# Kernel tuning notes

Measured on AMD Instinct MI355X. Metric: run time of the kernel, lower is better.

## Reference

```python
import jax, jax.numpy as jnp
import numpy as np

N_NODES = 100000
N_EDGES = 1600000
N_GRAPHS = 5000
NODE_DIM = 16
EDGE_DIM = 16
HID = 20


def setup_inputs() -> dict:
    key = jax.random.key(0)
    ks = jax.random.split(key, 12)
    edge_index = jax.random.randint(ks[0], (2, N_EDGES), 0, N_NODES)
    node_attr = jax.random.normal(ks[1], (N_NODES, NODE_DIM), dtype=jnp.float32)
    edge_attr = jax.random.normal(ks[2], (N_EDGES, EDGE_DIM), dtype=jnp.float32)
    batch = jnp.sort(jax.random.randint(ks[3], (N_NODES,), 0, N_GRAPHS))
    s = 0.1
    W_msg = jax.random.normal(ks[4], (2 * NODE_DIM + EDGE_DIM, HID), dtype=jnp.float32) * s
    b_msg = jnp.zeros((HID,), dtype=jnp.float32)
    W1 = jax.random.normal(ks[5], (HID, 10), dtype=jnp.float32) * s
    b1 = jnp.zeros((10,), dtype=jnp.float32)
    W2 = jax.random.normal(ks[6], (10, 10), dtype=jnp.float32) * s
    b2 = jnp.zeros((10,), dtype=jnp.float32)
    W3 = jax.random.normal(ks[7], (10, 1), dtype=jnp.float32) * s
    b3 = jnp.zeros((1,), dtype=jnp.float32)
    return {"edge_index": edge_index, "node_attr": node_attr, "edge_attr": edge_attr,
            "batch": batch, "W_msg": W_msg, "b_msg": b_msg, "W1": W1, "b1": b1,
            "W2": W2, "b2": b2, "W3": W3, "b3": b3}


def reference(edge_index, node_attr, edge_attr, batch,
              W_msg, b_msg, W1, b1, W2, b2, W3, b3):
    src, dst = edge_index[0], edge_index[1]
    # MPL_1: gather -> linear -> relu -> scatter-sum to destination nodes
    feats = jnp.concatenate([node_attr[src], node_attr[dst], edge_attr], axis=-1)  # [E, 48]
    msg = jax.nn.relu(feats @ W_msg + b_msg)  # [E, 20]
    x = jax.ops.segment_sum(msg, dst, num_segments=N_NODES)  # [N, 20]
    # node MLP + graph pooling (segment_coo sum over batch) + graph MLP
    x = jax.nn.relu(x @ W1 + b1)  # [N, 10]
    g = jax.ops.segment_sum(x, batch, num_segments=N_GRAPHS)  # [G, 10]
    g = jax.nn.relu(g @ W2 + b2)
    return g @ W3 + b3  # [G, 1]
```

## Files before the change

### kernel.cpp

```cpp
#include <hip/hip_runtime.h>

constexpr int NN = 100000;
constexpr int NE = 1600000;
constexpr int NG = 5000;
constexpr int BKT = 64;
constexpr int NBKT = (NN + BKT - 1) / BKT;
constexpr int NB = 128;
constexpr int CHUNK = NE / NB;

typedef float v2f __attribute__((ext_vector_type(2)));

constexpr size_t OFF_G  = 0;
constexpr size_t OFF_BH = 50048;
constexpr size_t OFF_ST = OFF_BH + (size_t)NB * NBKT;
constexpr size_t OFF_PM = OFF_ST + NBKT + 1;

__global__ __launch_bounds__(256) void k_hist(const int* __restrict__ ei,
                                              int* __restrict__ bh,
                                              float* __restrict__ g) {
  __shared__ int lh[NBKT];
  for (int i = threadIdx.x; i < NBKT; i += 256) lh[i] = 0;
  __syncthreads();
  const int* dstp = ei + NE;
  int s = blockIdx.x * CHUNK;
  for (int i = s + threadIdx.x; i < s + CHUNK; i += 256)
    atomicAdd(&lh[dstp[i] >> 6], 1);
  int gid = blockIdx.x * 256 + threadIdx.x;
  if (gid < 12500) ((float4*)g)[gid] = make_float4(0.f, 0.f, 0.f, 0.f);
  __syncthreads();
  int* out = bh + (size_t)blockIdx.x * NBKT;
  for (int k = threadIdx.x; k < NBKT; k += 256) out[k] = lh[k];
}

__global__ __launch_bounds__(256) void k_btot(const int* __restrict__ bh,
                                              int* __restrict__ starts) {
  int k = blockIdx.x * 256 + threadIdx.x;
  if (k >= NBKT) return;
  int tot = 0;
  for (int b = 0; b < NB; b += 4) {
    int a0 = bh[(size_t)(b    ) * NBKT + k];
    int a1 = bh[(size_t)(b + 1) * NBKT + k];
    int a2 = bh[(size_t)(b + 2) * NBKT + k];
    int a3 = bh[(size_t)(b + 3) * NBKT + k];
    tot += a0 + a1 + a2 + a3;
  }
  starts[k] = tot;
}

__global__ __launch_bounds__(1024) void k_sscan(int* __restrict__ starts) {
  __shared__ int s0[1024], s1[1024];
  int t = threadIdx.x;
  int k0 = 2 * t, k1 = 2 * t + 1;
  int tot0 = (k0 < NBKT) ? starts[k0] : 0;
  int tot1 = (k1 < NBKT) ? starts[k1] : 0;
  int ssum = tot0 + tot1;
  int* cur = s0; int* nxt = s1;
  cur[t] = ssum;
  __syncthreads();
  for (int off = 1; off < 1024; off <<= 1) {
    int v = cur[t];
    if (t >= off) v += cur[t - off];
    nxt[t] = v;
    __syncthreads();
    int* tmp = cur; cur = nxt; nxt = tmp;
  }
  int excl = cur[t] - ssum;
  if (k0 < NBKT) starts[k0] = excl;
  if (k1 <= NBKT) starts[k1] = excl + tot0;
}

__global__ __launch_bounds__(256) void k_bases(int* __restrict__ bh,
                                               const int* __restrict__ starts) {
  int k = blockIdx.x * 256 + threadIdx.x;
  if (k >= NBKT) return;
  int run = starts[k];
  for (int b = 0; b < NB; ++b) {
    size_t idx = (size_t)b * NBKT + k;
    int v = bh[idx];
    bh[idx] = run;
    run += v;
  }
}

__global__ __launch_bounds__(256) void k_scatter(const int* __restrict__ ei,
                                                 const int* __restrict__ bh,
                                                 int* __restrict__ perm) {
  __shared__ int base[NBKT];
  __shared__ int cnt[NBKT];
  const int* row = bh + (size_t)blockIdx.x * NBKT;
  for (int k = threadIdx.x; k < NBKT; k += 256) { base[k] = row[k]; cnt[k] = 0; }
  __syncthreads();
  const int* dstp = ei + NE;
  int s = blockIdx.x * CHUNK;
  for (int i = s + threadIdx.x; i < s + CHUNK; i += 256) {
    int d = dstp[i];
    int k = d >> 6;
    int r = atomicAdd(&cnt[k], 1);
    perm[base[k] + r] = i | ((d & 63) << 24);
  }
}

#define PK4(V, T) { \
  float4 wA = wt4[wrow + (T)];     \
  float4 wB = wt4[wrow + (T) + 1]; \
  a0 = __builtin_elementwise_fma(v2f{(V).x, (V).x}, v2f{wA.x, wA.y}, a0); \
  a1 = __builtin_elementwise_fma(v2f{(V).y, (V).y}, v2f{wA.z, wA.w}, a1); \
  a2 = __builtin_elementwise_fma(v2f{(V).z, (V).z}, v2f{wB.x, wB.y}, a2); \
  a3 = __builtin_elementwise_fma(v2f{(V).w, (V).w}, v2f{wB.z, wB.w}, a3); }

__global__ __launch_bounds__(512, 4) void k_edge(
    const int* __restrict__ ei,
    const float* __restrict__ nattr,
    const float* __restrict__ eattr,
    const float* __restrict__ Wm,
    const float* __restrict__ bm,
    const int* __restrict__ batch,
    const float* __restrict__ W1,
    const float* __restrict__ b1,
    const int* __restrict__ perm,
    const int* __restrict__ starts,
    float* __restrict__ g) {
  __shared__ float xt[20 * 65];
  __shared__ float gb[64 * 10];
  __shared__ float4 wt4[250];
  __shared__ int s_se[2];
  __shared__ int s_bmin;
  for (int i = threadIdx.x; i < 20 * 65; i += 512) xt[i] = 0.f;
  for (int i = threadIdx.x; i < 640; i += 512) gb[i] = 0.f;
  if (threadIdx.x < 240) {
    int i = threadIdx.x;
    int j = i / 24, t = i - j * 24, k = 2 * t;
    wt4[j * 25 + t] = make_float4(Wm[k * 20 + 2 * j],       Wm[k * 20 + 2 * j + 1],
                                  Wm[(k + 1) * 20 + 2 * j], Wm[(k + 1) * 20 + 2 * j + 1]);
  }
  if (threadIdx.x < 2) s_se[threadIdx.x] = starts[blockIdx.x + threadIdx.x];
  int nbase = blockIdx.x * BKT;
  if (threadIdx.x == 0) s_bmin = batch[nbase];
  __syncthreads();
  int is = s_se[0], ie = s_se[1];

  int wave = threadIdx.x >> 6;
  int lane = threadIdx.x & 63;
  int ep = lane / 10;
  int jp = lane - ep * 10;
  bool act = ep < 6;
  int epc = act ? ep : 0;

  v2f bj = {bm[2 * jp], bm[2 * jp + 1]};

  int base = is + wave * 6;
  int p0 = 0, p1 = 0, sv0 = 0;
  if (base < ie) {
    p0 = perm[min(base + epc, ie - 1)];
    sv0 = ei[p0 & 0xFFFFFF];
    p1 = (base + 48 < ie) ? perm[min(base + 48 + epc, ie - 1)] : p0;
  }
  while (base < ie) {
    int b2 = base + 96;
    int p2 = (b2 < ie) ? perm[min(b2 + epc, ie - 1)] : p1;
    int sN = (base + 48 < ie) ? ei[p1 & 0xFFFFFF] : sv0;

    const float4* pe = (const float4*)(eattr + (size_t)(p0 & 0xFFFFFF) * 16);
    const float4* ps = (const float4*)(nattr + (size_t)sv0 * 16);
    float4 e0 = pe[0], e1 = pe[1], e2 = pe[2], e3 = pe[3];
    float4 n0 = ps[0], n1 = ps[1], n2 = ps[2], n3 = ps[3];
    int dl = (p0 >> 24) & 63;
    const float4* pd = (const float4*)(nattr + (size_t)(nbase + dl) * 16);
    float4 u0 = pd[0], u1 = pd[1], u2 = pd[2], u3 = pd[3];

    int wrow = jp * 25;
    asm volatile("" : "+v"(wrow));

    v2f a0 = {0.f, 0.f}, a1 = {0.f, 0.f}, a2 = {0.f, 0.f}, a3 = {0.f, 0.f};
    PK4(n0, 0)  PK4(n1, 2)  PK4(n2, 4)  PK4(n3, 6)
    PK4(u0, 8)  PK4(u1, 10) PK4(u2, 12) PK4(u3, 14)
    PK4(e0, 16) PK4(e1, 18) PK4(e2, 20) PK4(e3, 22)
    v2f r = ((a0 + a1) + (a2 + a3)) + bj;

    bool valid = act && (base + epc < ie);
    float m0 = fmaxf(r.x, 0.f);
    float m1 = fmaxf(r.y, 0.f);
    if (valid && m0 > 0.f) atomicAdd(&xt[(2 * jp) * 65 + dl], m0);
    if (valid && m1 > 0.f) atomicAdd(&xt[(2 * jp + 1) * 65 + dl], m1);

    base += 48; p0 = p1; p1 = p2; sv0 = sN;
  }
  __syncthreads();

  int nn = min(BKT, NN - nbase);
  int bmin = s_bmin;
  if (threadIdx.x < 64 && (int)threadIdx.x < nn) {
    int node = threadIdx.x;
    float xi[20];
#pragma unroll
    for (int j = 0; j < 20; ++j) xi[j] = xt[j * 65 + node];
    float acc[10];
#pragma unroll
    for (int j = 0; j < 10; ++j) acc[j] = b1[j];
#pragma unroll
    for (int k = 0; k < 20; ++k) {
      float fk = xi[k];
#pragma unroll
      for (int j = 0; j < 10; ++j) acc[j] = fmaf(fk, W1[k * 10 + j], acc[j]);
    }
    int bn = batch[nbase + node];
    int d = bn - bmin;
    if (d < 64) {
#pragma unroll
      for (int j = 0; j < 10; ++j) {
        float m = fmaxf(acc[j], 0.f);
        if (m > 0.f) atomicAdd(&gb[d * 10 + j], m);
      }
    } else {
#pragma unroll
      for (int j = 0; j < 10; ++j) {
        float m = fmaxf(acc[j], 0.f);
        if (m > 0.f) unsafeAtomicAdd(&g[(size_t)bn * 10 + j], m);
      }
    }
  }
  __syncthreads();
  int glim = min(640, NG * 10 - bmin * 10);
  float* gp = g + (size_t)bmin * 10;
  for (int idx = threadIdx.x; idx < glim; idx += 512) {
    float v = gb[idx];
    if (v != 0.f) unsafeAtomicAdd(&gp[idx], v);
  }
}

__global__ __launch_bounds__(256) void k_graph(
    const float* __restrict__ g,
    const float* __restrict__ W2, const float* __restrict__ b2,
    const float* __restrict__ W3, const float* __restrict__ b3,
    float* __restrict__ out) {
  int i = blockIdx.x * 256 + threadIdx.x;
  if (i >= NG) return;
  float gi[10];
  const float2* pg = (const float2*)(g + (size_t)i * 10);
#pragma unroll
  for (int k = 0; k < 5; ++k) { float2 v = pg[k]; gi[2*k] = v.x; gi[2*k+1] = v.y; }
  float o = b3[0];
#pragma unroll
  for (int j = 0; j < 10; ++j) {
    float a = b2[j];
#pragma unroll
    for (int k = 0; k < 10; ++k) a = fmaf(gi[k], W2[k * 10 + j], a);
    o = fmaf(fmaxf(a, 0.f), W3[j], o);
  }
  out[i] = o;
}

extern "C" void kernel_launch(void* const* d_in, const int* in_sizes, int n_in,
                              void* d_out, int out_size, void* d_ws, size_t ws_size,
                              hipStream_t stream) {
  const int*   ei    = (const int*)  d_in[0];
  const float* nattr = (const float*)d_in[1];
  const float* eattr = (const float*)d_in[2];
  const int*   batch = (const int*)  d_in[3];
  const float* Wm    = (const float*)d_in[4];
  const float* bm    = (const float*)d_in[5];
  const float* W1    = (const float*)d_in[6];
  const float* b1    = (const float*)d_in[7];
  const float* W2    = (const float*)d_in[8];
  const float* b2    = (const float*)d_in[9];
  const float* W3    = (const float*)d_in[10];
  const float* b3    = (const float*)d_in[11];

  float* g      = (float*)d_ws + OFF_G;
  int*   bh     = (int*)d_ws + OFF_BH;
  int*   starts = (int*)d_ws + OFF_ST;
  int*   perm   = (int*)d_ws + OFF_PM;

  constexpr int SCAN_BLKS = (NBKT + 255) / 256;

  k_hist   <<<NB, 256, 0, stream>>>(ei, bh, g);
  k_btot   <<<SCAN_BLKS, 256, 0, stream>>>(bh, starts);
  k_sscan  <<<1, 1024, 0, stream>>>(starts);
  k_bases  <<<SCAN_BLKS, 256, 0, stream>>>(bh, starts);
  k_scatter<<<NB, 256, 0, stream>>>(ei, bh, perm);
  k_edge   <<<NBKT, 512, 0, stream>>>(ei, nattr, eattr, Wm, bm, batch, W1, b1,
                                      perm, starts, g);
  k_graph  <<<(NG + 255) / 256, 256, 0, stream>>>(g, W2, b2, W3, b3, (float*)d_out);
}
```

Measured before the change: 379.4 us.

## Stage edge and source features cooperatively through LDS with deeper prefetch

```diff
diff --git a/kernel.cpp b/kernel.cpp
--- a/kernel.cpp
+++ b/kernel.cpp
@@ -108,7 +108,7 @@
   a2 = __builtin_elementwise_fma(v2f{(V).z, (V).z}, v2f{wB.x, wB.y}, a2); \
   a3 = __builtin_elementwise_fma(v2f{(V).w, (V).w}, v2f{wB.z, wB.w}, a3); }
 
-__global__ __launch_bounds__(512, 4) void k_edge(
+__global__ __launch_bounds__(512, 3) void k_edge(
     const int* __restrict__ ei,
     const float* __restrict__ nattr,
     const float* __restrict__ eattr,
@@ -123,24 +123,31 @@
   __shared__ float xt[20 * 65];
   __shared__ float gb[64 * 10];
   __shared__ float4 wt4[250];
+  __shared__ float4 us4[64 * 5];
+  __shared__ float4 feat[8 * 54];
   __shared__ int s_se[2];
   __shared__ int s_bmin;
-  for (int i = threadIdx.x; i < 20 * 65; i += 512) xt[i] = 0.f;
-  for (int i = threadIdx.x; i < 640; i += 512) gb[i] = 0.f;
-  if (threadIdx.x < 240) {
-    int i = threadIdx.x;
-    int j = i / 24, t = i - j * 24, k = 2 * t;
+  int tid = threadIdx.x;
+  for (int i = tid; i < 20 * 65; i += 512) xt[i] = 0.f;
+  for (int i = tid; i < 640; i += 512) gb[i] = 0.f;
+  if (tid < 240) {
+    int j = tid / 24, t = tid - j * 24, k = 2 * t;
     wt4[j * 25 + t] = make_float4(Wm[k * 20 + 2 * j],       Wm[k * 20 + 2 * j + 1],
                                   Wm[(k + 1) * 20 + 2 * j], Wm[(k + 1) * 20 + 2 * j + 1]);
   }
-  if (threadIdx.x < 2) s_se[threadIdx.x] = starts[blockIdx.x + threadIdx.x];
   int nbase = blockIdx.x * BKT;
-  if (threadIdx.x == 0) s_bmin = batch[nbase];
+  if (tid < 256) {
+    int dl = tid >> 2, part = tid & 3;
+    int row = min(nbase + dl, NN - 1);
+    us4[dl * 5 + part] = ((const float4*)nattr)[(size_t)row * 4 + part];
+  }
+  if (tid < 2) s_se[tid] = starts[blockIdx.x + tid];
+  if (tid == 0) s_bmin = batch[nbase];
   __syncthreads();
   int is = s_se[0], ie = s_se[1];
 
-  int wave = threadIdx.x >> 6;
-  int lane = threadIdx.x & 63;
+  int wave = tid >> 6;
+  int lane = tid & 63;
   int ep = lane / 10;
   int jp = lane - ep * 10;
   bool act = ep < 6;
@@ -148,28 +155,48 @@
 
   v2f bj = {bm[2 * jp], bm[2 * jp + 1]};
 
+  int ce = lane >> 3, cpart = lane & 7;
+  bool ldr = lane < 48;
+  int esrc = (ldr ? ce : 0) * 10;
+  int fbase = wave * 54;
+
   int base = is + wave * 6;
-  int p0 = 0, p1 = 0, sv0 = 0;
+  int p0 = 0, p1 = 0, p2 = 0, svn = 0;
+  float4 st = make_float4(0.f, 0.f, 0.f, 0.f);
   if (base < ie) {
     p0 = perm[min(base + epc, ie - 1)];
-    sv0 = ei[p0 & 0xFFFFFF];
     p1 = (base + 48 < ie) ? perm[min(base + 48 + epc, ie - 1)] : p0;
+    p2 = (base + 96 < ie) ? perm[min(base + 96 + epc, ie - 1)] : p1;
+    int sv0 = ei[p0 & 0xFFFFFF];
+    svn     = ei[p1 & 0xFFFFFF];
+    int pp = __shfl(p0, esrc);
+    int ss = __shfl(sv0, esrc);
+    if (ldr) {
+      const float4* a = (cpart < 4)
+          ? ((const float4*)eattr) + (size_t)(pp & 0xFFFFFF) * 4 + cpart
+          : ((const float4*)nattr) + (size_t)ss * 4 + (cpart - 4);
+      st = *a;
+    }
   }
   while (base < ie) {
-    int b2 = base + 96;
-    int p2 = (b2 < ie) ? perm[min(b2 + epc, ie - 1)] : p1;
-    int sN = (base + 48 < ie) ? ei[p1 & 0xFFFFFF] : sv0;
-
-    const float4* pe = (const float4*)(eattr + (size_t)(p0 & 0xFFFFFF) * 16);
-    const float4* ps = (const float4*)(nattr + (size_t)sv0 * 16);
-    float4 e0 = pe[0], e1 = pe[1], e2 = pe[2], e3 = pe[3];
-    float4 n0 = ps[0], n1 = ps[1], n2 = ps[2], n3 = ps[3];
+    if (ldr) feat[fbase + ce * 9 + cpart] = st;
+    int pp = __shfl(p1, esrc);
+    int ss = __shfl(svn, esrc);
+    int p3 = (base + 144 < ie) ? perm[min(base + 144 + epc, ie - 1)] : p2;
+    int svn2 = ei[p2 & 0xFFFFFF];
+    if (ldr) {
+      const float4* a = (cpart < 4)
+          ? ((const float4*)eattr) + (size_t)(pp & 0xFFFFFF) * 4 + cpart
+          : ((const float4*)nattr) + (size_t)ss * 4 + (cpart - 4);
+      st = *a;
+    }
     int dl = (p0 >> 24) & 63;
-    const float4* pd = (const float4*)(nattr + (size_t)(nbase + dl) * 16);
-    float4 u0 = pd[0], u1 = pd[1], u2 = pd[2], u3 = pd[3];
-
     int wrow = jp * 25;
     asm volatile("" : "+v"(wrow));
+    int frow = fbase + ep * 9;
+    float4 e0 = feat[frow + 0], e1 = feat[frow + 1], e2 = feat[frow + 2], e3 = feat[frow + 3];
+    float4 n0 = feat[frow + 4], n1 = feat[frow + 5], n2 = feat[frow + 6], n3 = feat[frow + 7];
+    float4 u0 = us4[dl * 5 + 0], u1 = us4[dl * 5 + 1], u2 = us4[dl * 5 + 2], u3 = us4[dl * 5 + 3];
 
     v2f a0 = {0.f, 0.f}, a1 = {0.f, 0.f}, a2 = {0.f, 0.f}, a3 = {0.f, 0.f};
     PK4(n0, 0)  PK4(n1, 2)  PK4(n2, 4)  PK4(n3, 6)
@@ -183,14 +210,14 @@
     if (valid && m0 > 0.f) atomicAdd(&xt[(2 * jp) * 65 + dl], m0);
     if (valid && m1 > 0.f) atomicAdd(&xt[(2 * jp + 1) * 65 + dl], m1);
 
-    base += 48; p0 = p1; p1 = p2; sv0 = sN;
+    base += 48; p0 = p1; p1 = p2; p2 = p3; svn = svn2;
   }
   __syncthreads();
 
   int nn = min(BKT, NN - nbase);
   int bmin = s_bmin;
-  if (threadIdx.x < 64 && (int)threadIdx.x < nn) {
-    int node = threadIdx.x;
+  if (tid < 64 && tid < nn) {
+    int node = tid;
     float xi[20];
 #pragma unroll
     for (int j = 0; j < 20; ++j) xi[j] = xt[j * 65 + node];
@@ -222,7 +249,7 @@
   __syncthreads();
   int glim = min(640, NG * 10 - bmin * 10);
   float* gp = g + (size_t)bmin * 10;
-  for (int idx = threadIdx.x; idx < glim; idx += 512) {
+  for (int idx = tid; idx < glim; idx += 512) {
     float v = gb[idx];
     if (v != 0.f) unsafeAtomicAdd(&gp[idx], v);
   }
```

After: 397.3 us. 4.7% more time.
